# Performance work log

Hardware: AMD Instinct MI355X
Metric: run time of the kernel (lower is better)

## Reference

```python
import jax, jax.numpy as jnp
import numpy as np

GRID = 16            # spp grid (init kwarg)
K_MAX = 32           # max entries per cell (xy.shape[1] - 3)
B = 64               # number of graphs in batch
N_PER = 2048         # nodes per graph (equal-sized graphs)
D = 256              # input_dim
R = GRID * GRID      # max valid cell-rows per graph; valid rows come first


def setup_inputs() -> dict:
    key = jax.random.key(0)
    rng = np.random.default_rng(0)
    # xy layout per row: [grid_row, grid_col, count, idx_0 ... idx_{K_MAX-1}]
    # rows beyond the first R per graph are sentinel (-1) => original code breaks.
    xy = np.zeros((B, N_PER, 3 + K_MAX), dtype=np.int64)
    xy[:, :, 0] = -1
    cells = np.argsort(rng.random((B, R)), axis=1)  # unique cell per valid row
    xy[:, :R, 0] = cells // GRID
    xy[:, :R, 1] = cells % GRID
    xy[:, :R, 2] = rng.integers(1, K_MAX + 1, size=(B, R))
    xy[:, :R, 3:] = rng.integers(0, N_PER, size=(B, R, K_MAX))
    features = jax.random.normal(key, (B * N_PER, D), dtype=jnp.float32)
    nodes_per_graph = jnp.full((B,), N_PER, dtype=jnp.int64)
    return {"features": features,
            "xy": jnp.asarray(xy.reshape(B * N_PER, 3 + K_MAX)),
            "nodes_per_graph": nodes_per_graph}


def reference(features, xy, nodes_per_graph):
    Bn = nodes_per_graph.shape[0]
    n_per = features.shape[0] // Bn
    d = features.shape[1]
    F = features.reshape(Bn, n_per, d)                 # graph-local node feats
    xyb = xy.reshape(Bn, n_per, -1)[:, :R]             # valid rows are first R
    rows, cols, counts = xyb[..., 0], xyb[..., 1], xyb[..., 2]
    inds = xyb[..., 3:]                                # [B, R, K]
    valid = rows >= 0
    # per-cell gather of node features: [B, R, K, D]
    gathered = jax.vmap(lambda f, i: f[i])(F, inds)
    k_mask = (jnp.arange(inds.shape[-1])[None, None, :] < counts[..., None])
    denom = jnp.maximum(counts, 1).astype(features.dtype)[..., None]
    # mean readout over the first `count` entries
    pooled = (gathered * k_mask[..., None].astype(features.dtype)).sum(axis=2) / denom
    # scatter into dense grid; invalid rows routed to a dummy slot
    cell = jnp.where(valid, rows * GRID + cols, GRID * GRID)
    out = jnp.zeros((Bn, GRID * GRID + 1, d), features.dtype)
    out = out.at[jnp.arange(Bn)[:, None], cell].set(pooled)
    out = out[:, :GRID * GRID].reshape(Bn, GRID, GRID, d)
    return jnp.transpose(out, (0, 3, 1, 2))            # [B, D, GRID, GRID]
```

## Files before the change

kernel.cpp:

```cpp
#include <hip/hip_runtime.h>

#define GRIDN   16
#define KMAX    32
#define NPER    2048
#define DFEAT   256
#define RCELLS  256
#define XYS     35

__global__ __launch_bounds__(256, 4) void spp_pool_phase1(
    const float* __restrict__ F,
    const int*   __restrict__ xy,
    float*       __restrict__ ws,
    int B)
{
    int bx = blockIdx.x;
    int b, chunk;
    if ((B & 7) == 0) {
        int xcd = bx & 7;
        int s   = bx >> 3;
        b     = xcd * (B >> 3) + (s >> 7);
        chunk = s & 127;
    } else {
        b     = bx >> 7;
        chunk = bx & 127;
    }

    int tid  = threadIdx.x;
    int wv   = tid >> 6;
    int lane = tid & 63;
    int rowi = wv >> 1;
    int kh   = wv & 1;
    int r    = chunk * 2 + rowi;

    __shared__ float part[2][DFEAT];

    const int* xr = xy + ((size_t)b * NPER + r) * XYS;
    int row = xr[0];
    int col = xr[1];
    int cnt = (row >= 0) ? xr[2] : 0;
    if (cnt > KMAX) cnt = KMAX;
    int vidx = xr[3 + kh * 16 + (lane & 15)];

    const float4* Fb4 = (const float4*)(F + (size_t)b * NPER * DFEAT);
    float4 acc = make_float4(0.f, 0.f, 0.f, 0.f);
    int base = kh * 16;
    #pragma unroll
    for (int rr = 0; rr < 2; ++rr) {
        int kb = base + rr * 8;
        if (kb < cnt) {
            int   idx[8];
            float w[8];
            #pragma unroll
            for (int j = 0; j < 8; ++j) {
                int raw = __shfl(vidx, rr * 8 + j);
                bool ok = (kb + j) < cnt;
                idx[j] = ok ? raw : 0;
                w[j]   = ok ? 1.f : 0.f;
            }
            float4 f[8];
            #pragma unroll
            for (int j = 0; j < 8; ++j)
                f[j] = Fb4[(size_t)idx[j] * 64 + lane];
            #pragma unroll
            for (int j = 0; j < 8; ++j) {
                acc.x += w[j] * f[j].x;
                acc.y += w[j] * f[j].y;
                acc.z += w[j] * f[j].z;
                acc.w += w[j] * f[j].w;
            }
        }
    }

    if (kh == 1) *(float4*)&part[rowi][lane * 4] = acc;
    __syncthreads();
    if (kh == 0 && row >= 0) {
        float4 p = *(const float4*)&part[rowi][lane * 4];
        float inv = 1.f / (float)(cnt > 0 ? cnt : 1);
        float4 res;
        res.x = (acc.x + p.x) * inv;
        res.y = (acc.y + p.y) * inv;
        res.z = (acc.z + p.z) * inv;
        res.w = (acc.w + p.w) * inv;
        int cell = row * GRIDN + col;
        *(float4*)(ws + ((size_t)b * RCELLS + cell) * DFEAT + lane * 4) = res;
    }
}

__global__ __launch_bounds__(256, 4) void spp_pool_phase2(
    const float* __restrict__ ws,
    float*       __restrict__ out,
    int B)
{
    int bx = blockIdx.x;
    int b, c0;
    if ((B & 7) == 0) {
        int xcd = bx & 7;
        int s   = bx >> 3;
        b  = xcd * (B >> 3) + (s >> 2);
        c0 = (s & 3) * 64;
    } else {
        b  = bx >> 2;
        c0 = (bx & 3) * 64;
    }
    int d = threadIdx.x;

    float v[64];
    const float* wsb = ws + (size_t)b * RCELLS * DFEAT + d;
    #pragma unroll
    for (int i = 0; i < 64; ++i)
        v[i] = wsb[(size_t)(c0 + i) * DFEAT];

    float* ob = out + (size_t)b * DFEAT * RCELLS + (size_t)d * RCELLS + c0;
    #pragma unroll
    for (int i = 0; i < 16; ++i) {
        float4 q = make_float4(v[4*i], v[4*i+1], v[4*i+2], v[4*i+3]);
        *(float4*)(ob + 4 * i) = q;
    }
}

extern "C" void kernel_launch(void* const* d_in, const int* in_sizes, int n_in,
                              void* d_out, int out_size, void* d_ws, size_t ws_size,
                              hipStream_t stream) {
    const float* F   = (const float*)d_in[0];
    const int*   xy  = (const int*)d_in[1];
    float*       out = (float*)d_out;
    float*       ws  = (float*)d_ws;
    int B = in_sizes[2];

    hipLaunchKernelGGL(spp_pool_phase1, dim3(B * 128), dim3(256), 0, stream,
                       F, xy, ws, B);
    hipLaunchKernelGGL(spp_pool_phase2, dim3(B * 4), dim3(256), 0, stream,
                       ws, out, B);
}
```

Before: 214.8 us.

## Assign one wavefront per cell row, drop LDS reduction, use readlane indices

Phase 1 now gives each wavefront a full cell row (four rows per block) instead of splitting the K entries across two waves and reducing through shared memory. The xy row is loaded once per wave and the indices are broadcast with readlane. Up to 16 gathers are issued per batch before accumulating, and the shared memory buffer and __syncthreads are removed. Launch bounds rise to 6 and the grid is halved. The trade-off is less parallelism per row and more registers per thread for the 16-deep gather batches.

```diff
diff --git a/kernel.cpp b/kernel.cpp
--- a/kernel.cpp
+++ b/kernel.cpp
@@ -7,7 +7,11 @@
 #define RCELLS  256
 #define XYS     35
 
-__global__ __launch_bounds__(256, 4) void spp_pool_phase1(
+__device__ __forceinline__ void add4(float4& a, const float4& b) {
+    a.x += b.x; a.y += b.y; a.z += b.z; a.w += b.w;
+}
+
+__global__ __launch_bounds__(256, 6) void spp_pool_phase1(
     const float* __restrict__ F,
     const int*   __restrict__ xy,
     float*       __restrict__ ws,
@@ -18,72 +22,65 @@
     if ((B & 7) == 0) {
         int xcd = bx & 7;
         int s   = bx >> 3;
-        b     = xcd * (B >> 3) + (s >> 7);
-        chunk = s & 127;
+        b     = xcd * (B >> 3) + (s >> 6);
+        chunk = s & 63;
     } else {
-        b     = bx >> 7;
-        chunk = bx & 127;
+        b     = bx >> 6;
+        chunk = bx & 63;
     }
 
     int tid  = threadIdx.x;
     int wv   = tid >> 6;
     int lane = tid & 63;
-    int rowi = wv >> 1;
-    int kh   = wv & 1;
-    int r    = chunk * 2 + rowi;
-
-    __shared__ float part[2][DFEAT];
+    int r    = chunk * 4 + wv;
 
     const int* xr = xy + ((size_t)b * NPER + r) * XYS;
-    int row = xr[0];
-    int col = xr[1];
-    int cnt = (row >= 0) ? xr[2] : 0;
+    int hv = xr[lane < XYS ? lane : 0];
+
+    int row = __builtin_amdgcn_readlane(hv, 0);
+    int col = __builtin_amdgcn_readlane(hv, 1);
+    int cnt = __builtin_amdgcn_readlane(hv, 2);
+    if (row < 0) return;
     if (cnt > KMAX) cnt = KMAX;
-    int vidx = xr[3 + kh * 16 + (lane & 15)];
 
     const float4* Fb4 = (const float4*)(F + (size_t)b * NPER * DFEAT);
     float4 acc = make_float4(0.f, 0.f, 0.f, 0.f);
-    int base = kh * 16;
-    #pragma unroll
-    for (int rr = 0; rr < 2; ++rr) {
-        int kb = base + rr * 8;
-        if (kb < cnt) {
-            int   idx[8];
-            float w[8];
-            #pragma unroll
-            for (int j = 0; j < 8; ++j) {
-                int raw = __shfl(vidx, rr * 8 + j);
-                bool ok = (kb + j) < cnt;
-                idx[j] = ok ? raw : 0;
-                w[j]   = ok ? 1.f : 0.f;
-            }
-            float4 f[8];
-            #pragma unroll
-            for (int j = 0; j < 8; ++j)
-                f[j] = Fb4[(size_t)idx[j] * 64 + lane];
-            #pragma unroll
-            for (int j = 0; j < 8; ++j) {
-                acc.x += w[j] * f[j].x;
-                acc.y += w[j] * f[j].y;
-                acc.z += w[j] * f[j].z;
-                acc.w += w[j] * f[j].w;
-            }
+
+    {
+        float4 f[16];
+        #pragma unroll
+        for (int j = 0; j < 16; ++j) {
+            int raw = __builtin_amdgcn_readlane(hv, 3 + j);
+            int idx = (j < cnt) ? raw : 0;
+            f[j] = Fb4[(size_t)idx * 64 + lane];
+        }
+        #pragma unroll
+        for (int j = 0; j < 16; ++j) {
+            float w = (j < cnt) ? 1.f : 0.f;
+            acc.x += w * f[j].x; acc.y += w * f[j].y;
+            acc.z += w * f[j].z; acc.w += w * f[j].w;
+        }
+    }
+    if (cnt > 16) {
+        float4 f[16];
+        #pragma unroll
+        for (int j = 0; j < 16; ++j) {
+            int raw = __builtin_amdgcn_readlane(hv, 19 + j);
+            int idx = (16 + j < cnt) ? raw : 0;
+            f[j] = Fb4[(size_t)idx * 64 + lane];
+        }
+        #pragma unroll
+        for (int j = 0; j < 16; ++j) {
+            float w = (16 + j < cnt) ? 1.f : 0.f;
+            acc.x += w * f[j].x; acc.y += w * f[j].y;
+            acc.z += w * f[j].z; acc.w += w * f[j].w;
         }
     }
 
-    if (kh == 1) *(float4*)&part[rowi][lane * 4] = acc;
-    __syncthreads();
-    if (kh == 0 && row >= 0) {
-        float4 p = *(const float4*)&part[rowi][lane * 4];
-        float inv = 1.f / (float)(cnt > 0 ? cnt : 1);
-        float4 res;
-        res.x = (acc.x + p.x) * inv;
-        res.y = (acc.y + p.y) * inv;
-        res.z = (acc.z + p.z) * inv;
-        res.w = (acc.w + p.w) * inv;
-        int cell = row * GRIDN + col;
-        *(float4*)(ws + ((size_t)b * RCELLS + cell) * DFEAT + lane * 4) = res;
-    }
+    float inv = 1.f / (float)(cnt > 0 ? cnt : 1);
+    float4 res = make_float4(acc.x * inv, acc.y * inv, acc.z * inv, acc.w * inv);
+    int cell = row * GRIDN + col;
+    *(float4*)(ws + ((size_t)b * RCELLS + cell) * DFEAT + lane * 4) = res;
 }
 
 __global__ __launch_bounds__(256, 4) void spp_pool_phase2(
@@ -127,7 +124,7 @@
     float*       ws  = (float*)d_ws;
     int B = in_sizes[2];
 
-    hipLaunchKernelGGL(spp_pool_phase1, dim3(B * 128), dim3(256), 0, stream,
+    hipLaunchKernelGGL(spp_pool_phase1, dim3(B * 64), dim3(256), 0, stream,
                        F, xy, ws, B);
     hipLaunchKernelGGL(spp_pool_phase2, dim3(B * 4), dim3(256), 0, stream,
                        ws, out, B);
```

Result: no change. 215.9 us (+0.5%).
